# Performance work log

Measured on AMD Instinct MI355X. Metric: run time of the kernel, lower is better.

The kernel has to match this reference:

```python
import jax, jax.numpy as jnp
import numpy as np

B, S, DIM, H = 2, 2048, 512, 8  # batch, seq_len, model dim, num_heads


def setup_inputs() -> dict:
    key = jax.random.key(0)
    ks = jax.random.split(key, 8)
    s = 0.02
    return {
        "queries": jax.random.normal(ks[0], (B, S, DIM), dtype=jnp.float32),
        "keys": jax.random.normal(ks[1], (B, S, DIM), dtype=jnp.float32),
        "Wq": jax.random.normal(ks[2], (DIM, DIM), dtype=jnp.float32) * s,
        "bq": jax.random.normal(ks[3], (DIM,), dtype=jnp.float32) * s,
        "Wk": jax.random.normal(ks[4], (DIM, DIM), dtype=jnp.float32) * s,
        "bk": jax.random.normal(ks[5], (DIM,), dtype=jnp.float32) * s,
        "Wv": jax.random.normal(ks[6], (DIM, DIM), dtype=jnp.float32) * s,
        "bv": jax.random.normal(ks[7], (DIM,), dtype=jnp.float32) * s,
        "causality": 1,
    }


def _split_heads(x):
    # torch: cat(chunk(x, H, dim=2), dim=0): [B,S,D] -> [H*B, S, d], head-major
    b, s, dmod = x.shape
    d = dmod // H
    return x.reshape(b, s, H, d).transpose(2, 0, 1, 3).reshape(H * b, s, d)


def reference(queries, keys, Wq, bq, Wk, bk, Wv, bv, causality):
    b, sq, dim = queries.shape
    sk = keys.shape[1]
    d = dim // H

    Q = queries @ Wq.T + bq
    K = keys @ Wk.T + bk
    V = keys @ Wv.T + bv
    Q_, K_, V_ = _split_heads(Q), _split_heads(K), _split_heads(V)  # [H*B, S, d]

    scores = jnp.einsum("nqd,nkd->nqk", Q_, K_) / jnp.sqrt(jnp.float32(d))

    # key padding mask from raw keys: sign(sum |keys|) -> [B,Sk] -> [H*B,1,Sk]
    key_masks = jnp.sign(jnp.sum(jnp.abs(keys), axis=-1))
    key_masks = jnp.tile(key_masks, (H, 1))[:, None, :]
    scores = jnp.where(key_masks == 0, -jnp.inf, scores)

    if causality:
        tril = jnp.tril(jnp.ones((sq, sk), dtype=bool))
        scores = jnp.where(tril[None, :, :], scores, -jnp.inf)

    attn = jax.nn.softmax(scores, axis=-1)
    attn = jnp.nan_to_num(attn, nan=0.0, posinf=0.0, neginf=0.0)

    # query padding mask: [B,Sq] -> [H*B,Sq,1], multiplicative
    query_masks = jnp.sign(jnp.sum(jnp.abs(queries), axis=-1))
    query_masks = jnp.tile(query_masks, (H, 1))[:, :, None]
    attn = attn * query_masks

    # attention_weights: stack H chunks along dim 1 -> [B, H, Sq, Sk]
    attention_weights = attn.reshape(H, b, sq, sk).transpose(1, 0, 2, 3)

    # dropout in eval mode = identity
    out = jnp.einsum("nqk,nkd->nqd", attn, V_)  # [H*B, Sq, d]
    # merge heads back: cat(chunk(out, H, dim=0), dim=2)
    out = out.reshape(H, b, sq, d).transpose(1, 2, 0, 3).reshape(b, sq, dim)
    return out, attention_weights
```

## Files before the change

kernel.cpp:

```cpp
#include <hip/hip_runtime.h>
#include <math.h>

#define B_ 2
#define S_ 2048
#define DIM_ 512
#define H_ 8
#define DH_ 64

typedef __bf16 bf16x8 __attribute__((ext_vector_type(8)));
typedef float f32x4 __attribute__((ext_vector_type(4)));
typedef float vf4 __attribute__((ext_vector_type(4)));
typedef unsigned short ushort_t;
typedef ushort_t ushort8 __attribute__((ext_vector_type(8)));

__device__ __forceinline__ ushort_t f2bf(float f) {
    union { float f; unsigned u; } v; v.f = f;
    unsigned u = v.u;
    return (ushort_t)((u + 0x7FFFu + ((u >> 16) & 1u)) >> 16);
}
__device__ __forceinline__ float bf2f(ushort_t u) {
    union { unsigned u; float f; } v; v.u = ((unsigned)u) << 16;
    return v.f;
}

__global__ __launch_bounds__(256) void convert_kernel(
    const float* __restrict__ q, const float* __restrict__ k,
    const float* __restrict__ wq, const float* __restrict__ wk,
    const float* __restrict__ wv,
    ushort_t* qbf, ushort_t* kbf, ushort_t* wqb, ushort_t* wkb, ushort_t* wvb)
{
    const float* src; ushort_t* dst; int n;
    switch (blockIdx.y) {
        case 0: src = q;  dst = qbf; n = B_ * S_ * DIM_; break;
        case 1: src = k;  dst = kbf; n = B_ * S_ * DIM_; break;
        case 2: src = wq; dst = wqb; n = DIM_ * DIM_; break;
        case 3: src = wk; dst = wkb; n = DIM_ * DIM_; break;
        default: src = wv; dst = wvb; n = DIM_ * DIM_; break;
    }
    int i4 = blockIdx.x * 256 + threadIdx.x;
    if (i4 * 4 >= n) return;
    float4 v = ((const float4*)src)[i4];
    ushort4 o;
    o.x = f2bf(v.x); o.y = f2bf(v.y); o.z = f2bf(v.z); o.w = f2bf(v.w);
    ((ushort4*)dst)[i4] = o;
}

__global__ __launch_bounds__(256) void proj_mfma_kernel(
    const ushort_t* __restrict__ Qin, const ushort_t* __restrict__ Kin,
    const ushort_t* __restrict__ Wqb, const float* __restrict__ bq,
    const ushort_t* __restrict__ Wkb, const float* __restrict__ bk,
    const ushort_t* __restrict__ Wvb, const float* __restrict__ bv,
    ushort_t* __restrict__ Qh, ushort_t* __restrict__ Kh, ushort_t* __restrict__ Vt)
{
    __shared__ float T[128][68];

    const int which = blockIdx.z;
    const ushort_t* A = (which == 0) ? Qin : Kin;
    const ushort_t* W = (which == 0) ? Wqb : (which == 1 ? Wkb : Wvb);
    const float* bias = (which == 0) ? bq : (which == 1 ? bk : bv);

    const int r0 = blockIdx.x * 128;
    const int h  = blockIdx.y;
    const int c0 = h * DH_;
    const int tid = threadIdx.x;
    const int w = tid >> 6, l = tid & 63;
    const int lr = l & 15, lg = l >> 4;

    f32x4 acc[2][4] = {};
    const ushort_t* arow0 = A + (size_t)(r0 + w * 32 + lr) * DIM_ + lg * 8;
    const ushort_t* arow1 = arow0 + (size_t)16 * DIM_;
    const ushort_t* wrow0 = W + (size_t)(c0 + lr) * DIM_ + lg * 8;

#pragma unroll 4
    for (int ks = 0; ks < DIM_ / 32; ++ks) {
        bf16x8 a0 = *(const bf16x8*)(arow0 + ks * 32);
        bf16x8 a1 = *(const bf16x8*)(arow1 + ks * 32);
#pragma unroll
        for (int ct = 0; ct < 4; ++ct) {
            bf16x8 bfr = *(const bf16x8*)(wrow0 + (size_t)ct * 16 * DIM_ + ks * 32);
            acc[0][ct] = __builtin_amdgcn_mfma_f32_16x16x32_bf16(a0, bfr, acc[0][ct], 0, 0, 0);
            acc[1][ct] = __builtin_amdgcn_mfma_f32_16x16x32_bf16(a1, bfr, acc[1][ct], 0, 0, 0);
        }
    }

    const int bb = r0 >> 11;
    const int s0 = r0 & (S_ - 1);
    const int n = h * B_ + bb;

    if (which < 2) {
        ushort_t* OUT = (which == 0) ? Qh : Kh;
#pragma unroll
        for (int rg = 0; rg < 2; ++rg) {
#pragma unroll
            for (int ct = 0; ct < 4; ++ct) {
                int d = ct * 16 + lr;
                float bi = bias[c0 + d];
#pragma unroll
                for (int reg = 0; reg < 4; ++reg) {
                    int s = s0 + w * 32 + rg * 16 + lg * 4 + reg;
                    OUT[((size_t)n * S_ + s) * DH_ + d] = f2bf(acc[rg][ct][reg] + bi);
                }
            }
        }
    } else {
#pragma unroll
        for (int rg = 0; rg < 2; ++rg) {
#pragma unroll
            for (int ct = 0; ct < 4; ++ct) {
                int d = ct * 16 + lr;
                float bi = bias[c0 + d];
#pragma unroll
                for (int reg = 0; reg < 4; ++reg)
                    T[w * 32 + rg * 16 + lg * 4 + reg][d] = acc[rg][ct][reg] + bi;
            }
        }
        __syncthreads();
        int d = tid & 63, sc = tid >> 6;
        ushort8 o[4];
#pragma unroll
        for (int i = 0; i < 32; ++i)
            ((ushort_t*)o)[i] = f2bf(T[sc * 32 + i][d]);
        ushort8* dst = (ushort8*)(Vt + ((size_t)n * DH_ + d) * S_ + s0 + sc * 32);
        dst[0] = o[0]; dst[1] = o[1]; dst[2] = o[2]; dst[3] = o[3];
    }
}

__global__ __launch_bounds__(64) void attn_core_kernel(
    const ushort_t* __restrict__ Qh, const ushort_t* __restrict__ Kh,
    const ushort_t* __restrict__ Vt, const int* __restrict__ causp,
    float* __restrict__ outp, float* __restrict__ attnw,
    float* __restrict__ inv_ws)
{
    __shared__ ushort_t Pscr[16][40];

    const int bid = blockIdx.x;
    const int x = bid & 7, i = bid >> 3;
    const int n  = x * 2 + (i & 1);
    const int qt = 127 - (i >> 1);
    const int h = n / B_, b = n % B_;
    const int q0 = qt * 16;
    const int l = threadIdx.x;
    const int lr = l & 15, lg = l >> 4;
    const int causal = causp[0];

    const int kend = causal ? (((q0 + 47) >> 5) << 5) : S_;
    const int q_g = q0 + lr;

    float* attrow = attnw + ((size_t)((b * H_ + h) * S_ + q0)) * S_;
    ushort_t* prow = (ushort_t*)(attrow + (size_t)lr * S_);

    const ushort_t* qrow = Qh + ((size_t)n * S_ + q0 + lr) * DH_ + lg * 8;
    bf16x8 qa0 = *(const bf16x8*)(qrow);
    bf16x8 qa1 = *(const bf16x8*)(qrow + 32);
    const ushort_t* Kbase = Kh + (size_t)n * S_ * DH_;
    const ushort_t* Vbase = Vt + (size_t)n * DH_ * S_;

    float pl = 0.f;
    f32x4 oacc[4] = {};
    {
        const ushort_t* kr = Kbase + (size_t)lr * DH_ + lg * 8;
        bf16x8 ka0 = *(const bf16x8*)(kr);
        bf16x8 ka1 = *(const bf16x8*)(kr + 32);
        bf16x8 kb0 = *(const bf16x8*)(kr + 16 * DH_);
        bf16x8 kb1 = *(const bf16x8*)(kr + 16 * DH_ + 32);
        bf16x8 va[4];
#pragma unroll
        for (int dt = 0; dt < 4; ++dt)
            va[dt] = *(const bf16x8*)(Vbase + (size_t)(dt * 16 + lr) * S_ + lg * 8);

        for (int kc = 0; kc < kend; kc += 32) {
            const int kn = (kc + 32 < kend) ? kc + 32 : kc;
            const ushort_t* krn = Kbase + (size_t)(kn + lr) * DH_ + lg * 8;
            bf16x8 na0 = *(const bf16x8*)(krn);
            bf16x8 na1 = *(const bf16x8*)(krn + 32);
            bf16x8 nb0 = *(const bf16x8*)(krn + 16 * DH_);
            bf16x8 nb1 = *(const bf16x8*)(krn + 16 * DH_ + 32);
            bf16x8 nva[4];
#pragma unroll
            for (int dt = 0; dt < 4; ++dt)
                nva[dt] = *(const bf16x8*)(Vbase + (size_t)(dt * 16 + lr) * S_ + kn + lg * 8);

            f32x4 a0 = {}, a1 = {};
            a0 = __builtin_amdgcn_mfma_f32_16x16x32_bf16(ka0, qa0, a0, 0, 0, 0);
            a0 = __builtin_amdgcn_mfma_f32_16x16x32_bf16(ka1, qa1, a0, 0, 0, 0);
            a1 = __builtin_amdgcn_mfma_f32_16x16x32_bf16(kb0, qa0, a1, 0, 0, 0);
            a1 = __builtin_amdgcn_mfma_f32_16x16x32_bf16(kb1, qa1, a1, 0, 0, 0);

            ushort4 u0, u1;
            const bool msk = causal && (kc + 32 >= kend);
#pragma unroll
            for (int reg = 0; reg < 4; ++reg) {
                float e0 = __expf(a0[reg] * 0.125f);
                float e1 = __expf(a1[reg] * 0.125f);
                if (msk) {
                    if (kc + lg * 4 + reg > q_g)      e0 = 0.f;
                    if (kc + 16 + lg * 4 + reg > q_g) e1 = 0.f;
                }
                pl += e0 + e1;
                __bf16 t0 = (__bf16)e0, t1 = (__bf16)e1;
                ((ushort_t*)&u0)[reg] = *(ushort_t*)&t0;
                ((ushort_t*)&u1)[reg] = *(ushort_t*)&t1;
            }
            *(ushort4*)&prow[kc + lg * 4]      = u0;
            *(ushort4*)&prow[kc + 16 + lg * 4] = u1;

            *(ushort4*)&Pscr[lr][lg * 4]      = u0;
            *(ushort4*)&Pscr[lr][16 + lg * 4] = u1;
            bf16x8 pa = *(const bf16x8*)&Pscr[lr][lg * 8];
#pragma unroll
            for (int dt = 0; dt < 4; ++dt)
                oacc[dt] = __builtin_amdgcn_mfma_f32_16x16x32_bf16(pa, va[dt], oacc[dt], 0, 0, 0);

            ka0 = na0; ka1 = na1; kb0 = nb0; kb1 = nb1;
#pragma unroll
            for (int dt = 0; dt < 4; ++dt) va[dt] = nva[dt];
        }
    }

    pl += __shfl_xor(pl, 16);
    pl += __shfl_xor(pl, 32);
    const float inv = 1.f / pl;
    if (lg == 0) inv_ws[n * S_ + q0 + lr] = inv;

    float inv_r[4];
#pragma unroll
    for (int reg = 0; reg < 4; ++reg)
        inv_r[reg] = __shfl(inv, lg * 4 + reg, 64);
#pragma unroll
    for (int dt = 0; dt < 4; ++dt)
#pragma unroll
        for (int reg = 0; reg < 4; ++reg) {
            int qq = q0 + lg * 4 + reg;
            outp[((size_t)b * S_ + qq) * DIM_ + h * DH_ + dt * 16 + lr] =
                oacc[dt][reg] * inv_r[reg];
        }
}

__global__ __launch_bounds__(256) void attn_stream_kernel(
    const float* __restrict__ inv_ws, const int* __restrict__ causp,
    float* __restrict__ attnw)
{
    const int bid = blockIdx.x;
    const int x = bid & 7;
    const int ridx = bid >> 3;
    const int n = x * 2 + (ridx & 1);
    const int q = ridx >> 1;
    const int h = n / B_, b = n % B_;
    const int causal = causp[0];
    const int kend = causal ? (((((q >> 4) << 4) + 47) >> 5) << 5) : S_;
    const int t = threadIdx.x;
    const int c = t * 8;

    float* ar = attnw + ((size_t)(b * H_ + h) * S_ + q) * S_;
    const float inv = inv_ws[n * S_ + q];

    ushort8 v = {};
    if (c < kend) v = *(const ushort8*)((const ushort_t*)ar + c);
    __syncthreads();

    vf4 o0 = {0.f, 0.f, 0.f, 0.f}, o1 = {0.f, 0.f, 0.f, 0.f};
    if (c < kend) {
        o0.x = bf2f(v[0]) * inv; o0.y = bf2f(v[1]) * inv;
        o0.z = bf2f(v[2]) * inv; o0.w = bf2f(v[3]) * inv;
        o1.x = bf2f(v[4]) * inv; o1.y = bf2f(v[5]) * inv;
        o1.z = bf2f(v[6]) * inv; o1.w = bf2f(v[7]) * inv;
    }
    *(vf4*)&ar[c] = o0;
    *(vf4*)&ar[c + 4] = o1;
}

extern "C" void kernel_launch(void* const* d_in, const int* in_sizes, int n_in,
                              void* d_out, int out_size, void* d_ws, size_t ws_size,
                              hipStream_t stream) {
    const float* queries = (const float*)d_in[0];
    const float* keys    = (const float*)d_in[1];
    const float* Wq = (const float*)d_in[2];
    const float* bq = (const float*)d_in[3];
    const float* Wk = (const float*)d_in[4];
    const float* bk = (const float*)d_in[5];
    const float* Wv = (const float*)d_in[6];
    const float* bv = (const float*)d_in[7];
    const int*   caus = (const int*)d_in[8];

    char* ws = (char*)d_ws;
    ushort_t* Qin_bf = (ushort_t*)ws;  ws += (size_t)B_*S_*DIM_*2;
    ushort_t* Kin_bf = (ushort_t*)ws;  ws += (size_t)B_*S_*DIM_*2;
    ushort_t* Wqb = (ushort_t*)ws;     ws += (size_t)DIM_*DIM_*2;
    ushort_t* Wkb = (ushort_t*)ws;     ws += (size_t)DIM_*DIM_*2;
    ushort_t* Wvb = (ushort_t*)ws;     ws += (size_t)DIM_*DIM_*2;
    ushort_t* Qh = (ushort_t*)ws;      ws += (size_t)H_*B_*S_*DH_*2;
    ushort_t* Kh = (ushort_t*)ws;      ws += (size_t)H_*B_*S_*DH_*2;
    ushort_t* Vt = (ushort_t*)ws;      ws += (size_t)H_*B_*DH_*S_*2;
    float* inv_ws = (float*)ws;        ws += (size_t)H_*B_*S_*4;

    float* outp  = (float*)d_out;
    float* attnw = outp + (size_t)B_ * S_ * DIM_;

    convert_kernel<<<dim3(2048, 5), 256, 0, stream>>>(
        queries, keys, Wq, Wk, Wv, Qin_bf, Kin_bf, Wqb, Wkb, Wvb);

    proj_mfma_kernel<<<dim3(32, 8, 3), 256, 0, stream>>>(
        Qin_bf, Kin_bf, Wqb, bq, Wkb, bk, Wvb, bv, Qh, Kh, Vt);

    attn_core_kernel<<<2048, 64, 0, stream>>>(Qh, Kh, Vt, caus, outp, attnw, inv_ws);

    attn_stream_kernel<<<H_ * B_ * S_, 256, 0, stream>>>(inv_ws, caus, attnw);
}
```

Baseline: 177.9 us.

## Split attention key range across four waves per block with LDS reduction

The attention core kernel now runs four waves per 16-query tile, each taking a contiguous quarter of the key range. Partial row sums and output accumulators are reduced through shared memory before normalising and writing the output. The unnormalised probability store is reorganised so each lane writes a contiguous 16-byte chunk of one row, staged through LDS. The cross-iteration register prefetch of K/V is dropped, and the extra LDS and a block barrier are added. The aim is to shorten the serial per-block loop and improve latency hiding.

```diff
diff --git a/kernel.cpp b/kernel.cpp
--- a/kernel.cpp
+++ b/kernel.cpp
@@ -125,13 +125,15 @@
     }
 }
 
-__global__ __launch_bounds__(64) void attn_core_kernel(
+__global__ __launch_bounds__(256, 6) void attn_core_kernel(
     const ushort_t* __restrict__ Qh, const ushort_t* __restrict__ Kh,
     const ushort_t* __restrict__ Vt, const int* __restrict__ causp,
     float* __restrict__ outp, float* __restrict__ attnw,
     float* __restrict__ inv_ws)
 {
-    __shared__ ushort_t Pscr[16][40];
+    __shared__ ushort_t Pscr[4][16][40];
+    __shared__ float o_lds[4][16][68];
+    __shared__ float sums_lds[4][16];
 
     const int bid = blockIdx.x;
     const int x = bid & 7, i = bid >> 3;
@@ -139,15 +141,19 @@
     const int qt = 127 - (i >> 1);
     const int h = n / B_, b = n % B_;
     const int q0 = qt * 16;
-    const int l = threadIdx.x;
+    const int tid = threadIdx.x;
+    const int w = tid >> 6, l = tid & 63;
     const int lr = l & 15, lg = l >> 4;
     const int causal = causp[0];
 
     const int kend = causal ? (((q0 + 47) >> 5) << 5) : S_;
     const int q_g = q0 + lr;
 
+    const int ck = (((kend >> 2) + 31) >> 5) << 5;
+    const int wstart = w * ck;
+    const int wend   = (wstart + ck < kend) ? wstart + ck : kend;
+
     float* attrow = attnw + ((size_t)((b * H_ + h) * S_ + q0)) * S_;
-    ushort_t* prow = (ushort_t*)(attrow + (size_t)lr * S_);
 
     const ushort_t* qrow = Qh + ((size_t)n * S_ + q0 + lr) * DH_ + lg * 8;
     bf16x8 qa0 = *(const bf16x8*)(qrow);
@@ -155,10 +161,12 @@
     const ushort_t* Kbase = Kh + (size_t)n * S_ * DH_;
     const ushort_t* Vbase = Vt + (size_t)n * DH_ * S_;
 
+    const int r4 = l >> 2, c4 = l & 3;
+
     float pl = 0.f;
     f32x4 oacc[4] = {};
-    {
-        const ushort_t* kr = Kbase + (size_t)lr * DH_ + lg * 8;
+    for (int kc = wstart; kc < wend; kc += 32) {
+        const ushort_t* kr = Kbase + (size_t)(kc + lr) * DH_ + lg * 8;
         bf16x8 ka0 = *(const bf16x8*)(kr);
         bf16x8 ka1 = *(const bf16x8*)(kr + 32);
         bf16x8 kb0 = *(const bf16x8*)(kr + 16 * DH_);
@@ -166,74 +174,71 @@
         bf16x8 va[4];
 #pragma unroll
         for (int dt = 0; dt < 4; ++dt)
-            va[dt] = *(const bf16x8*)(Vbase + (size_t)(dt * 16 + lr) * S_ + lg * 8);
-
-        for (int kc = 0; kc < kend; kc += 32) {
-            const int kn = (kc + 32 < kend) ? kc + 32 : kc;
-            const ushort_t* krn = Kbase + (size_t)(kn + lr) * DH_ + lg * 8;
-            bf16x8 na0 = *(const bf16x8*)(krn);
-            bf16x8 na1 = *(const bf16x8*)(krn + 32);
-            bf16x8 nb0 = *(const bf16x8*)(krn + 16 * DH_);
-            bf16x8 nb1 = *(const bf16x8*)(krn + 16 * DH_ + 32);
-            bf16x8 nva[4];
-#pragma unroll
-            for (int dt = 0; dt < 4; ++dt)
-                nva[dt] = *(const bf16x8*)(Vbase + (size_t)(dt * 16 + lr) * S_ + kn + lg * 8);
-
-            f32x4 a0 = {}, a1 = {};
-            a0 = __builtin_amdgcn_mfma_f32_16x16x32_bf16(ka0, qa0, a0, 0, 0, 0);
-            a0 = __builtin_amdgcn_mfma_f32_16x16x32_bf16(ka1, qa1, a0, 0, 0, 0);
-            a1 = __builtin_amdgcn_mfma_f32_16x16x32_bf16(kb0, qa0, a1, 0, 0, 0);
-            a1 = __builtin_amdgcn_mfma_f32_16x16x32_bf16(kb1, qa1, a1, 0, 0, 0);
-
-            ushort4 u0, u1;
-            const bool msk = causal && (kc + 32 >= kend);
-#pragma unroll
-            for (int reg = 0; reg < 4; ++reg) {
-                float e0 = __expf(a0[reg] * 0.125f);
-                float e1 = __expf(a1[reg] * 0.125f);
-                if (msk) {
-                    if (kc + lg * 4 + reg > q_g)      e0 = 0.f;
-                    if (kc + 16 + lg * 4 + reg > q_g) e1 = 0.f;
-                }
-                pl += e0 + e1;
-                __bf16 t0 = (__bf16)e0, t1 = (__bf16)e1;
-                ((ushort_t*)&u0)[reg] = *(ushort_t*)&t0;
-                ((ushort_t*)&u1)[reg] = *(ushort_t*)&t1;
+            va[dt] = *(const bf16x8*)(Vbase + (size_t)(dt * 16 + lr) * S_ + kc + lg * 8);
+
+        f32x4 a0 = {}, a1 = {};
+        a0 = __builtin_amdgcn_mfma_f32_16x16x32_bf16(ka0, qa0, a0, 0, 0, 0);
+        a0 = __builtin_amdgcn_mfma_f32_16x16x32_bf16(ka1, qa1, a0, 0, 0, 0);
+        a1 = __builtin_amdgcn_mfma_f32_16x16x32_bf16(kb0, qa0, a1, 0, 0, 0);
+        a1 = __builtin_amdgcn_mfma_f32_16x16x32_bf16(kb1, qa1, a1, 0, 0, 0);
+
+        ushort4 u0, u1;
+        const bool msk = causal && (kc + 32 >= kend);
+#pragma unroll
+        for (int reg = 0; reg < 4; ++reg) {
+            float e0 = __expf(a0[reg] * 0.125f);
+            float e1 = __expf(a1[reg] * 0.125f);
+            if (msk) {
+                if (kc + lg * 4 + reg > q_g)      e0 = 0.f;
+                if (kc + 16 + lg * 4 + reg > q_g) e1 = 0.f;
             }
-            *(ushort4*)&prow[kc + lg * 4]      = u0;
-            *(ushort4*)&prow[kc + 16 + lg * 4] = u1;
-
-            *(ushort4*)&Pscr[lr][lg * 4]      = u0;
-            *(ushort4*)&Pscr[lr][16 + lg * 4] = u1;
-            bf16x8 pa = *(const bf16x8*)&Pscr[lr][lg * 8];
-#pragma unroll
-            for (int dt = 0; dt < 4; ++dt)
-                oacc[dt] = __builtin_amdgcn_mfma_f32_16x16x32_bf16(pa, va[dt], oacc[dt], 0, 0, 0);
-
-            ka0 = na0; ka1 = na1; kb0 = nb0; kb1 = nb1;
-#pragma unroll
-            for (int dt = 0; dt < 4; ++dt) va[dt] = nva[dt];
+            pl += e0 + e1;
+            __bf16 t0 = (__bf16)e0, t1 = (__bf16)e1;
+            ((ushort_t*)&u0)[reg] = *(ushort_t*)&t0;
+            ((ushort_t*)&u1)[reg] = *(ushort_t*)&t1;
         }
+
+        *(ushort4*)&Pscr[w][lr][lg * 4]      = u0;
+        *(ushort4*)&Pscr[w][lr][16 + lg * 4] = u1;
+
+        ushort8 srow = *(const ushort8*)&Pscr[w][r4][c4 * 8];
+        *(ushort8*)((ushort_t*)(attrow + (size_t)r4 * S_) + kc + c4 * 8) = srow;
+
+        bf16x8 pa = *(const bf16x8*)&Pscr[w][lr][lg * 8];
+#pragma unroll
+        for (int dt = 0; dt < 4; ++dt)
+            oacc[dt] = __builtin_amdgcn_mfma_f32_16x16x32_bf16(pa, va[dt], oacc[dt], 0, 0, 0);
     }
 
     pl += __shfl_xor(pl, 16);
     pl += __shfl_xor(pl, 32);
-    const float inv = 1.f / pl;
-    if (lg == 0) inv_ws[n * S_ + q0 + lr] = inv;
+    if (lg == 0) sums_lds[w][lr] = pl;
+
+#pragma unroll
+    for (int dt = 0; dt < 4; ++dt)
+#pragma unroll
+        for (int reg = 0; reg < 4; ++reg)
+            o_lds[w][lg * 4 + reg][dt * 16 + lr] = oacc[dt][reg];
+
+    __syncthreads();
 
     float inv_r[4];
 #pragma unroll
-    for (int reg = 0; reg < 4; ++reg)
-        inv_r[reg] = __shfl(inv, lg * 4 + reg, 64);
-#pragma unroll
-    for (int dt = 0; dt < 4; ++dt)
-#pragma unroll
-        for (int reg = 0; reg < 4; ++reg) {
-            int qq = q0 + lg * 4 + reg;
-            outp[((size_t)b * S_ + qq) * DIM_ + h * DH_ + dt * 16 + lr] =
-                oacc[dt][reg] * inv_r[reg];
-        }
+    for (int reg = 0; reg < 4; ++reg) {
+        int row = lg * 4 + reg;
+        inv_r[reg] = 1.f / (sums_lds[0][row] + sums_lds[1][row] +
+                            sums_lds[2][row] + sums_lds[3][row]);
+    }
+    if (w == 0 && lg == 0)
+        inv_ws[n * S_ + q0 + lr] = 1.f / (sums_lds[0][lr] + sums_lds[1][lr] +
+                                          sums_lds[2][lr] + sums_lds[3][lr]);
+#pragma unroll
+    for (int reg = 0; reg < 4; ++reg) {
+        int row = lg * 4 + reg;
+        float v = o_lds[0][row][w * 16 + lr] + o_lds[1][row][w * 16 + lr] +
+                  o_lds[2][row][w * 16 + lr] + o_lds[3][row][w * 16 + lr];
+        outp[((size_t)b * S_ + q0 + row) * DIM_ + h * DH_ + w * 16 + lr] = v * inv_r[reg];
+    }
 }
 
 __global__ __launch_bounds__(256) void attn_stream_kernel(
@@ -302,7 +307,7 @@
     proj_mfma_kernel<<<dim3(32, 8, 3), 256, 0, stream>>>(
         Qin_bf, Kin_bf, Wqb, bq, Wkb, bk, Wvb, bv, Qh, Kh, Vt);
 
-    attn_core_kernel<<<2048, 64, 0, stream>>>(Qh, Kh, Vt, caus, outp, attnw, inv_ws);
+    attn_core_kernel<<<2048, 256, 0, stream>>>(Qh, Kh, Vt, caus, outp, attnw, inv_ws);
 
     attn_stream_kernel<<<H_ * B_ * S_, 256, 0, stream>>>(inv_ws, caus, attnw);
 }
```

Result: no change. 175.9 us (-1.1%).
